# Kernel tuning notes

Hardware: AMD Instinct MI355X
Metric: run time of the kernel (lower is better)

## Reference

```python
import jax, jax.numpy as jnp
import numpy as np

# Dimensions: B point clouds of S points each, C channels, H heads of dim D
B, S, C, H, D = 8, 2048, 128, 4, 32
EPS = 1e-5  # GroupNorm eps (torch default)


def setup_inputs() -> dict:
    key = jax.random.key(0)
    ks = jax.random.split(key, 3)
    x = jax.random.normal(ks[0], (B, S, C), dtype=jnp.float32)
    # GroupNorm(num_groups=1) affine params (per-channel)
    gamma = jnp.ones((C,), dtype=jnp.float32)
    beta = jnp.zeros((C,), dtype=jnp.float32)
    # to_qkv: 1x1 Minkowski conv == linear, no bias; output = 3*H*D channels
    w_qkv = jax.random.normal(ks[1], (3 * H * D, C), dtype=jnp.float32) * 0.02
    # to_out: 1x1 conv with bias, H*D -> C
    w_out = jax.random.normal(ks[2], (C, H * D), dtype=jnp.float32) * 0.02
    b_out = jnp.zeros((C,), dtype=jnp.float32)
    return {"x": x, "gamma": gamma, "beta": beta, "w_qkv": w_qkv,
            "w_out": w_out, "b_out": b_out}


def reference(x, gamma, beta, w_qkv, w_out, b_out):
    scale = D ** -0.5
    # GroupNorm(num_groups=1) applied per cloud over ALL channels and points
    mu = jnp.mean(x, axis=(1, 2), keepdims=True)
    var = jnp.var(x, axis=(1, 2), keepdims=True)
    nx = (x - mu) * jax.lax.rsqrt(var + EPS) * gamma + beta  # [B,S,C]
    # Pointwise qkv projection (no bias)
    qkv = jnp.einsum('bsc,fc->bsf', nx, w_qkv)  # [B,S,3*H*D]
    q, k, v = jnp.split(qkv, 3, axis=-1)
    q = q.reshape(B, S, H, D) * scale
    k = k.reshape(B, S, H, D)
    v = v.reshape(B, S, H, D)
    # Per-cloud multi-head self-attention (block-diagonal over clouds)
    attn = jax.nn.softmax(jnp.einsum('bihd,bjhd->bhij', q, k), axis=-1)  # [B,H,S,S]
    o = jnp.einsum('bhij,bjhd->bihd', attn, v).reshape(B, S, H * D)
    # Output projection (with bias) + residual
    return jnp.einsum('bsf,cf->bsc', o, w_out) + b_out + x
```

## Files before the change

### kernel.cpp

```cpp
#include <hip/hip_runtime.h>
#include <hip/hip_bf16.h>

#define B_ 8
#define S_ 2048
#define C_ 128
#define H_ 4
#define D_ 32
#define SC_ (S_*C_)
#define HD_ (H_*D_)

typedef short bf16x8 __attribute__((ext_vector_type(8)));
typedef float f32x4 __attribute__((ext_vector_type(4)));
union FragU { uint4 u; bf16x8 h; };

__device__ __forceinline__ unsigned short f2bf(float f) {
  __hip_bfloat16 h = __float2bfloat16(f);
  return *reinterpret_cast<unsigned short*>(&h);
}
__device__ __forceinline__ unsigned int pk2t(float a, float b) {
  union { float f; unsigned int u; } ua, ub;
  ua.f = a; ub.f = b;
  return (ua.u >> 16) | (ub.u & 0xffff0000u);
}
#define EXP2(x) __builtin_amdgcn_exp2f(x)

__global__ __launch_bounds__(256) void k_stats1(const float* __restrict__ x,
                                                const float* __restrict__ wqkv,
                                                const float* __restrict__ wout,
                                                float* __restrict__ part,
                                                unsigned short* __restrict__ wq_bf,
                                                unsigned short* __restrict__ wo_bf) {
  __shared__ float ssum[256], ssq[256];
  int b = blockIdx.x >> 5, sl = blockIdx.x & 31;
  int tid = threadIdx.x;
  int gid = blockIdx.x * 256 + tid;
  if (gid < 16384) {
    int e = gid * 4;
    const float4 u = (e < 49152) ? *(const float4*)(wqkv + e) : *(const float4*)(wout + e - 49152);
    unsigned short tv[4] = {f2bf(u.x), f2bf(u.y), f2bf(u.z), f2bf(u.w)};
    unsigned short* dst = (e < 49152) ? (wq_bf + e) : (wo_bf + e - 49152);
    *(uint2*)dst = *(uint2*)tv;
  }
  const float4* xp = (const float4*)(x + (size_t)b * SC_);
  float sum = 0.f, sq = 0.f;
  for (int i = sl * 2048 + tid; i < (sl + 1) * 2048; i += 256) {
    float4 u = xp[i];
    sum += u.x + u.y + u.z + u.w;
    sq  += u.x*u.x + u.y*u.y + u.z*u.z + u.w*u.w;
  }
  ssum[tid] = sum; ssq[tid] = sq;
  __syncthreads();
  for (int s = 128; s > 0; s >>= 1) {
    if (tid < s) { ssum[tid] += ssum[tid + s]; ssq[tid] += ssq[tid + s]; }
    __syncthreads();
  }
  if (tid == 0) { part[blockIdx.x * 2] = ssum[0]; part[blockIdx.x * 2 + 1] = ssq[0]; }
}

__global__ __launch_bounds__(512) void k_qkv(const float* __restrict__ x,
                                             const float* __restrict__ gamma,
                                             const float* __restrict__ beta,
                                             const unsigned short* __restrict__ wq_bf,
                                             const float* __restrict__ part,
                                             unsigned short* __restrict__ q_ws,
                                             unsigned short* __restrict__ k_ws,
                                             unsigned short* __restrict__ v_ws) {
  __shared__ __align__(16) unsigned short Nls[32][136];
  __shared__ float gs[128], bs[128];
  __shared__ float st2[2];
  const int tid = threadIdx.x;
  const int w = tid >> 6, l = tid & 63, g = l >> 4, i = l & 15;
  const int gr0 = blockIdx.x * 32;
  const int b = gr0 >> 11;
  if (tid < 128) { gs[tid] = gamma[tid]; bs[tid] = beta[tid]; }
  if (tid < 32) {
    float s1 = part[(b * 32 + tid) * 2];
    float s2 = part[(b * 32 + tid) * 2 + 1];
    #pragma unroll
    for (int m = 16; m >= 1; m >>= 1) { s1 += __shfl_xor(s1, m); s2 += __shfl_xor(s2, m); }
    if (tid == 0) {
      float mu = s1 / (float)SC_;
      float var = s2 / (float)SC_ - mu * mu;
      st2[0] = mu; st2[1] = rsqrtf(var + 1e-5f);
    }
  }
  __syncthreads();
  const float mu = st2[0], rstd = st2[1];
  {
    const float4* xp = (const float4*)(x + (size_t)gr0 * C_);
    #pragma unroll
    for (int t = 0; t < 2; ++t) {
      int e = tid + t * 512;
      float4 u = xp[e];
      int r = e >> 5, c0 = (e & 31) * 4;
      float4 gv = *(const float4*)&gs[c0];
      float4 bv = *(const float4*)&bs[c0];
      unsigned short tv[4] = {
        f2bf((u.x - mu) * rstd * gv.x + bv.x),
        f2bf((u.y - mu) * rstd * gv.y + bv.y),
        f2bf((u.z - mu) * rstd * gv.z + bv.z),
        f2bf((u.w - mu) * rstd * gv.w + bv.w)};
      *(uint2*)&Nls[r][c0] = *(uint2*)tv;
    }
  }
  __syncthreads();
  f32x4 acc[2][3];
  #pragma unroll
  for (int rt = 0; rt < 2; ++rt)
    #pragma unroll
    for (int n = 0; n < 3; ++n) acc[rt][n] = (f32x4){0.f,0.f,0.f,0.f};

  #pragma unroll
  for (int kk = 0; kk < 4; ++kk) {
    FragU bfr[3];
    #pragma unroll
    for (int n = 0; n < 3; ++n)
      bfr[n].u = *(const uint4*)(wq_bf + (size_t)((w * 3 + n) * 16 + i) * 128 + kk * 32 + 8 * g);
    FragU af[2];
    #pragma unroll
    for (int rt = 0; rt < 2; ++rt) af[rt].u = *(const uint4*)&Nls[rt * 16 + i][kk * 32 + 8 * g];
    #pragma unroll
    for (int n = 0; n < 3; ++n)
      #pragma unroll
      for (int rt = 0; rt < 2; ++rt)
        acc[rt][n] = __builtin_amdgcn_mfma_f32_16x16x32_bf16(af[rt].h, bfr[n].h, acc[rt][n], 0, 0, 0);
  }
  const float SCQ = 0.17677669529663687f * 1.4426950408889634f;
  const int base64 = ((blockIdx.x & 63) >> 1) * 64;
  const int odd32 = (blockIdx.x & 1) * 32;
  #pragma unroll
  for (int n = 0; n < 3; ++n) {
    int f = (w * 3 + n) * 16 + i;
    int which = f >> 7, fi = f & 127, h = fi >> 5, dd = fi & 31;
    #pragma unroll
    for (int rt = 0; rt < 2; ++rt) {
      #pragma unroll
      for (int r = 0; r < 4; ++r) {
        int s = (gr0 + rt * 16 + 4 * g + r) & (S_ - 1);
        if (which == 0) {
          q_ws[(((size_t)b * H_ + h) * S_ + s) * D_ + dd] = f2bf(acc[rt][n][r] * SCQ);
        } else if (which == 1) {
          k_ws[(((size_t)b * H_ + h) * S_ + s) * D_ + dd] = f2bf(acc[rt][n][r]);
        } else {
          int slot = odd32 + 8 * g + 4 * rt + r;
          v_ws[(((size_t)b * H_ + h) * D_ + dd) * S_ + base64 + slot] = f2bf(acc[rt][n][r]);
        }
      }
    }
  }
}

__global__ __launch_bounds__(256) void k_attn(const unsigned short* __restrict__ qg,
                                              const unsigned short* __restrict__ kg,
                                              const unsigned short* __restrict__ vg,
                                              unsigned short* __restrict__ og) {
  __shared__ __align__(16) unsigned short Kls[2][64][40];
  __shared__ __align__(16) unsigned short Vt[2][32][72];
  const int tid = threadIdx.x;
  const int w = tid >> 6, l = tid & 63;
  const int g = l >> 4, i = l & 15;
  const int qb = blockIdx.x, h = blockIdx.y, b = blockIdx.z;
  const size_t base = ((size_t)b * H_ + h) * (size_t)(S_ * D_);

  FragU qf;
  qf.u = *(const uint4*)(qg + base + (size_t)(qb * 64 + w * 16 + i) * D_ + 8 * g);
  FragU onef;
  onef.u = (uint4){0x3F803F80u, 0x3F803F80u, 0x3F803F80u, 0x3F803F80u};

  const int sr  = tid >> 2;
  const int sc4 = tid & 3;
  const int vr  = tid >> 3;
  const int vc  = tid & 7;
  const uint4* kp = (const uint4*)(kg + base);
  const unsigned short* vt = vg + base;

  f32x4 oac[2] = {{0.f,0.f,0.f,0.f},{0.f,0.f,0.f,0.f}};
  f32x4 sac = {0.f,0.f,0.f,0.f};

  *(uint4*)&Kls[0][sr][sc4 * 8] = kp[sr * 4 + sc4];
  *(uint4*)&Vt[0][vr][vc * 8] = *(const uint4*)(vt + (size_t)vr * S_ + vc * 8);

  for (int kt = 0; kt < 32; ++kt) {
    const int cur = kt & 1;
    __syncthreads();
    uint4 nk, nv;
    const bool pf = kt < 31;
    if (pf) {
      nk = kp[((kt + 1) * 64 + sr) * 4 + sc4];
      nv = *(const uint4*)(vt + (size_t)vr * S_ + (kt + 1) * 64 + vc * 8);
    }
    f32x4 sf[4];
    __builtin_amdgcn_s_setprio(1);
    #pragma unroll
    for (int n = 0; n < 4; ++n) {
      FragU kf; kf.u = *(const uint4*)&Kls[cur][n * 16 + i][8 * g];
      f32x4 z = {0.f, 0.f, 0.f, 0.f};
      sf[n] = __builtin_amdgcn_mfma_f32_16x16x32_bf16(kf.h, qf.h, z, 0, 0, 0);
    }
    __builtin_amdgcn_s_setprio(0);
    FragU pa0, pa1;
    pa0.u = (uint4){pk2t(EXP2(sf[0][0]), EXP2(sf[0][1])),
                    pk2t(EXP2(sf[0][2]), EXP2(sf[0][3])),
                    pk2t(EXP2(sf[1][0]), EXP2(sf[1][1])),
                    pk2t(EXP2(sf[1][2]), EXP2(sf[1][3]))};
    pa1.u = (uint4){pk2t(EXP2(sf[2][0]), EXP2(sf[2][1])),
                    pk2t(EXP2(sf[2][2]), EXP2(sf[2][3])),
                    pk2t(EXP2(sf[3][0]), EXP2(sf[3][1])),
                    pk2t(EXP2(sf[3][2]), EXP2(sf[3][3]))};
    __builtin_amdgcn_s_setprio(1);
    sac = __builtin_amdgcn_mfma_f32_16x16x32_bf16(pa0.h, onef.h, sac, 0, 0, 0);
    #pragma unroll
    for (int n = 0; n < 2; ++n) {
      FragU vf; vf.u = *(const uint4*)&Vt[cur][n * 16 + i][8 * g];
      oac[n] = __builtin_amdgcn_mfma_f32_16x16x32_bf16(pa0.h, vf.h, oac[n], 0, 0, 0);
    }
    sac = __builtin_amdgcn_mfma_f32_16x16x32_bf16(pa1.h, onef.h, sac, 0, 0, 0);
    #pragma unroll
    for (int n = 0; n < 2; ++n) {
      FragU vf; vf.u = *(const uint4*)&Vt[cur][n * 16 + i][32 + 8 * g];
      oac[n] = __builtin_amdgcn_mfma_f32_16x16x32_bf16(pa1.h, vf.h, oac[n], 0, 0, 0);
    }
    __builtin_amdgcn_s_setprio(0);
    if (pf) {
      *(uint4*)&Kls[cur ^ 1][sr][sc4 * 8] = nk;
      *(uint4*)&Vt[cur ^ 1][vr][vc * 8] = nv;
    }
  }
  #pragma unroll
  for (int n = 0; n < 2; ++n) {
    #pragma unroll
    for (int r = 0; r < 4; ++r) {
      size_t row = (size_t)qb * 64 + w * 16 + 4 * g + r;
      og[((size_t)b * S_ + row) * HD_ + h * D_ + n * 16 + i] = f2bf(oac[n][r] / sac[r]);
    }
  }
}

__global__ __launch_bounds__(512) void k_out(const unsigned short* __restrict__ o,
                                             const unsigned short* __restrict__ wo_bf,
                                             const float* __restrict__ bo,
                                             const float* __restrict__ x,
                                             float* __restrict__ out) {
  const int tid = threadIdx.x;
  const int w = tid >> 6, l = tid & 63, g = l >> 4, i = l & 15;
  const int gr0 = blockIdx.x * 32;
  const int c = w * 16 + i;
  f32x4 acc[2] = {{0,0,0,0},{0,0,0,0}};
  #pragma unroll
  for (int kk = 0; kk < 4; ++kk) {
    FragU bfr;
    bfr.u = *(const uint4*)(wo_bf + (size_t)c * HD_ + kk * 32 + 8 * g);
    #pragma unroll
    for (int rt = 0; rt < 2; ++rt) {
      FragU af;
      af.u = *(const uint4*)(o + (size_t)(gr0 + rt * 16 + i) * HD_ + kk * 32 + 8 * g);
      acc[rt] = __builtin_amdgcn_mfma_f32_16x16x32_bf16(af.h, bfr.h, acc[rt], 0, 0, 0);
    }
  }
  float bias = bo[c];
  #pragma unroll
  for (int rt = 0; rt < 2; ++rt) {
    #pragma unroll
    for (int r = 0; r < 4; ++r) {
      size_t idx = (size_t)(gr0 + rt * 16 + 4 * g + r) * C_ + c;
      out[idx] = acc[rt][r] + bias + x[idx];
    }
  }
}

extern "C" void kernel_launch(void* const* d_in, const int* in_sizes, int n_in,
                              void* d_out, int out_size, void* d_ws, size_t ws_size,
                              hipStream_t stream) {
  const float* x     = (const float*)d_in[0];
  const float* gamma = (const float*)d_in[1];
  const float* beta  = (const float*)d_in[2];
  const float* wqkv  = (const float*)d_in[3];
  const float* wout  = (const float*)d_in[4];
  const float* bout  = (const float*)d_in[5];
  float* out = (float*)d_out;

  float* part  = (float*)((char*)d_ws + 64);
  unsigned short* wq_bf = (unsigned short*)((char*)d_ws + 4096);
  unsigned short* wo_bf = wq_bf + 49152;
  unsigned short* q_ws = (unsigned short*)((char*)d_ws + 4096 + 98304 + 32768);
  const size_t per = (size_t)B_ * H_ * S_ * D_;
  unsigned short* k_ws = q_ws + per;
  unsigned short* v_ws = k_ws + per;
  unsigned short* o_ws = v_ws + per;

  hipLaunchKernelGGL(k_stats1, dim3(256), dim3(256), 0, stream, x, wqkv, wout, part, wq_bf, wo_bf);
  hipLaunchKernelGGL(k_qkv, dim3(512), dim3(512), 0, stream,
                     x, gamma, beta, wq_bf, part, q_ws, k_ws, v_ws);
  hipLaunchKernelGGL(k_attn, dim3(S_ / 64, H_, B_), dim3(256), 0, stream,
                     q_ws, k_ws, v_ws, o_ws);
  hipLaunchKernelGGL(k_out, dim3(512), dim3(512), 0, stream,
                     o_ws, wo_bf, bout, x, out);
}
```

Before: 63.69 us.

## Split attention KV range across two blocks with separate reduction kernel

Splits each attention block's key/value loop in two, so twice as many workgroups run concurrently. Each half writes unnormalized fp32 output and row sums to workspace, and a new reduction kernel combines them, normalizes and writes bf16. This targets low occupancy: the original grid has 1024 blocks of 256 threads. It costs an extra kernel launch and fp32 partial-result traffic. The bf16 packing also switches to a single byte-permute instruction.

```diff
diff --git a/kernel.cpp b/kernel.cpp
--- a/kernel.cpp
+++ b/kernel.cpp
@@ -20,7 +20,7 @@
 __device__ __forceinline__ unsigned int pk2t(float a, float b) {
   union { float f; unsigned int u; } ua, ub;
   ua.f = a; ub.f = b;
-  return (ua.u >> 16) | (ub.u & 0xffff0000u);
+  return __builtin_amdgcn_perm(ub.u, ua.u, 0x07060302u);
 }
 #define EXP2(x) __builtin_amdgcn_exp2f(x)
 
@@ -153,13 +153,15 @@
 __global__ __launch_bounds__(256) void k_attn(const unsigned short* __restrict__ qg,
                                               const unsigned short* __restrict__ kg,
                                               const unsigned short* __restrict__ vg,
-                                              unsigned short* __restrict__ og) {
+                                              float* __restrict__ o_part,
+                                              float* __restrict__ sc_part) {
   __shared__ __align__(16) unsigned short Kls[2][64][40];
   __shared__ __align__(16) unsigned short Vt[2][32][72];
   const int tid = threadIdx.x;
   const int w = tid >> 6, l = tid & 63;
   const int g = l >> 4, i = l & 15;
-  const int qb = blockIdx.x, h = blockIdx.y, b = blockIdx.z;
+  const int qb = blockIdx.x, h = blockIdx.y;
+  const int b = blockIdx.z >> 1, half = blockIdx.z & 1;
   const size_t base = ((size_t)b * H_ + h) * (size_t)(S_ * D_);
 
   FragU qf;
@@ -177,14 +179,15 @@
   f32x4 oac[2] = {{0.f,0.f,0.f,0.f},{0.f,0.f,0.f,0.f}};
   f32x4 sac = {0.f,0.f,0.f,0.f};
 
-  *(uint4*)&Kls[0][sr][sc4 * 8] = kp[sr * 4 + sc4];
-  *(uint4*)&Vt[0][vr][vc * 8] = *(const uint4*)(vt + (size_t)vr * S_ + vc * 8);
-
-  for (int kt = 0; kt < 32; ++kt) {
+  const int kt0 = half * 16, ktE = kt0 + 16;
+  *(uint4*)&Kls[0][sr][sc4 * 8] = kp[(kt0 * 64 + sr) * 4 + sc4];
+  *(uint4*)&Vt[0][vr][vc * 8] = *(const uint4*)(vt + (size_t)vr * S_ + kt0 * 64 + vc * 8);
+
+  for (int kt = kt0; kt < ktE; ++kt) {
     const int cur = kt & 1;
     __syncthreads();
     uint4 nk, nv;
-    const bool pf = kt < 31;
+    const bool pf = kt < ktE - 1;
     if (pf) {
       nk = kp[((kt + 1) * 64 + sr) * 4 + sc4];
       nv = *(const uint4*)(vt + (size_t)vr * S_ + (kt + 1) * 64 + vc * 8);
@@ -226,14 +229,32 @@
       *(uint4*)&Vt[cur ^ 1][vr][vc * 8] = nv;
     }
   }
-  #pragma unroll
-  for (int n = 0; n < 2; ++n) {
-    #pragma unroll
-    for (int r = 0; r < 4; ++r) {
-      size_t row = (size_t)qb * 64 + w * 16 + 4 * g + r;
-      og[((size_t)b * S_ + row) * HD_ + h * D_ + n * 16 + i] = f2bf(oac[n][r] / sac[r]);
-    }
-  }
+  const size_t rbase = (size_t)(b * H_ + h) * S_ + (size_t)qb * 64 + w * 16;
+  float* op = o_part + ((size_t)half * B_ * H_ * S_ + rbase) * D_;
+  float* sp = sc_part + (size_t)half * B_ * H_ * S_ + rbase;
+  #pragma unroll
+  for (int r = 0; r < 4; ++r) {
+    int row = 4 * g + r;
+    #pragma unroll
+    for (int n = 0; n < 2; ++n) op[(size_t)row * D_ + n * 16 + i] = oac[n][r];
+    if (i == 0) sp[row] = sac[r];
+  }
+}
+
+__global__ __launch_bounds__(256) void k_attn_red(const float* __restrict__ o_part,
+                                                  const float* __restrict__ sc_part,
+                                                  unsigned short* __restrict__ og) {
+  const int tid = threadIdx.x;
+  const int r = blockIdx.x * 32 + (tid >> 3);
+  const int dc = (tid & 7) * 4;
+  const size_t NR = (size_t)B_ * H_ * S_;
+  float4 o1 = *(const float4*)(o_part + (size_t)r * D_ + dc);
+  float4 o2 = *(const float4*)(o_part + (NR + r) * D_ + dc);
+  float inv = 1.0f / (sc_part[r] + sc_part[NR + r]);
+  unsigned short tv[4] = {f2bf((o1.x + o2.x) * inv), f2bf((o1.y + o2.y) * inv),
+                          f2bf((o1.z + o2.z) * inv), f2bf((o1.w + o2.w) * inv)};
+  int b = r >> 13, h = (r >> 11) & 3, s = r & 2047;
+  *(uint2*)(og + ((size_t)(b * S_ + s)) * HD_ + h * D_ + dc) = *(uint2*)tv;
 }
 
 __global__ __launch_bounds__(512) void k_out(const unsigned short* __restrict__ o,
@@ -287,12 +308,15 @@
   unsigned short* k_ws = q_ws + per;
   unsigned short* v_ws = k_ws + per;
   unsigned short* o_ws = v_ws + per;
+  float* o_part  = (float*)((char*)d_ws + (20u << 20));
+  float* sc_part = (float*)((char*)d_ws + (40u << 20));
 
   hipLaunchKernelGGL(k_stats1, dim3(256), dim3(256), 0, stream, x, wqkv, wout, part, wq_bf, wo_bf);
   hipLaunchKernelGGL(k_qkv, dim3(512), dim3(512), 0, stream,
                      x, gamma, beta, wq_bf, part, q_ws, k_ws, v_ws);
-  hipLaunchKernelGGL(k_attn, dim3(S_ / 64, H_, B_), dim3(256), 0, stream,
-                     q_ws, k_ws, v_ws, o_ws);
+  hipLaunchKernelGGL(k_attn, dim3(S_ / 64, H_, B_ * 2), dim3(256), 0, stream,
+                     q_ws, k_ws, v_ws, o_part, sc_part);
+  hipLaunchKernelGGL(k_attn_red, dim3(2048), dim3(256), 0, stream, o_part, sc_part, o_ws);
   hipLaunchKernelGGL(k_out, dim3(512), dim3(512), 0, stream,
                      o_ws, wo_bf, bout, x, out);
 }
```

Result: slower. 69.16 us (+8.6%).
